# Kernel tuning notes

Hardware: AMD Instinct MI355X
Metric: run time of the kernel (lower is better)

Reference implementation:

```python
import jax, jax.numpy as jnp
import numpy as np

def mish(x):
    return x * jnp.tanh(jax.nn.softplus(x))

def setup_inputs() -> dict:
    ANT, RF, DS, G, B = 64, 8, 8, 16, 4096
    BB_DIM = 2 * RF * DS      # 128
    RF_DIM = 2 * ANT * RF     # 1024
    key = jax.random.key(0)
    ks = jax.random.split(key, 10)
    def lin(kw, kb, i, o):
        lim = 1.0 / np.sqrt(i)
        W = jax.random.uniform(kw, (o, i), jnp.float32, -lim, lim)
        b = jax.random.uniform(kb, (o,), jnp.float32, -lim, lim)
        return W, b
    W_rfbb, b_rfbb = lin(ks[0], ks[1], RF_DIM, BB_DIM)
    W_rfrf, b_rfrf = lin(ks[2], ks[3], RF_DIM, RF_DIM)
    W_bbrf, b_bbrf = lin(ks[4], ks[5], BB_DIM, RF_DIM)
    W_bbbb, b_bbbb = lin(ks[6], ks[7], BB_DIM, BB_DIM)
    BB_feature = jax.random.normal(ks[8], (B, G, BB_DIM), jnp.float32)
    RF_feature = jax.random.normal(ks[9], (B, RF_DIM), jnp.float32)
    return {
        "BB_feature": BB_feature, "RF_feature": RF_feature,
        "W_rfbb": W_rfbb, "b_rfbb": b_rfbb,
        "W_rfrf": W_rfrf, "b_rfrf": b_rfrf,
        "W_bbrf": W_bbrf, "b_bbrf": b_bbrf,
        "W_bbbb": W_bbbb, "b_bbbb": b_bbbb,
    }

def reference(BB_feature, RF_feature, W_rfbb, b_rfbb, W_rfrf, b_rfrf, W_bbrf, b_bbrf, W_bbbb, b_bbbb):
    # mean over subcarrier-group dim
    BB_mean = jnp.mean(BB_feature, axis=-2)                      # [B, BB_DIM]
    RF_to_RF = mish(RF_feature @ W_rfrf.T + b_rfrf)              # [B, RF_DIM]
    RF_to_BB = mish(RF_feature @ W_rfbb.T + b_rfbb)              # [B, BB_DIM]
    BB_to_RF = mish(BB_mean @ W_bbrf.T + b_bbrf)                 # [B, RF_DIM]
    BB_to_BB = mish(jnp.einsum('bgi,oi->bgo', BB_feature, W_bbbb) + b_bbbb)  # [B, G, BB_DIM]
    new_RF = RF_to_RF + BB_to_RF
    new_BB = BB_to_BB + RF_to_BB[:, None, :]
    return (new_BB, new_RF)
```

## Files before the change

### kernel.cpp

```cpp
#include <hip/hip_runtime.h>
#include <hip/hip_bf16.h>

typedef __attribute__((ext_vector_type(8))) short short8;
typedef __attribute__((ext_vector_type(4))) float floatx4;

#define BDIM 128
#define RDIM 1024
#define NB   4096
#define NG   16
#define LDP  40
#define WSTR 136

__device__ __forceinline__ float mishf(float x) {
    float e = __expf(x);
    float t = e * (e + 2.0f);
    float r = x * (t / (t + 2.0f));
    return x > 20.0f ? x : r;
}

__device__ __forceinline__ short8 cvt8v(float4 f0, float4 f1) {
    union { __hip_bfloat162 h; unsigned u; } c0, c1, c2, c3;
    c0.h = __float22bfloat162_rn(make_float2(f0.x, f0.y));
    c1.h = __float22bfloat162_rn(make_float2(f0.z, f0.w));
    c2.h = __float22bfloat162_rn(make_float2(f1.x, f1.y));
    c3.h = __float22bfloat162_rn(make_float2(f1.z, f1.w));
    union { short8 s; unsigned u[4]; } r;
    r.u[0] = c0.u; r.u[1] = c1.u; r.u[2] = c2.u; r.u[3] = c3.u;
    return r.s;
}

#define MFMA(a, b, c) __builtin_amdgcn_mfma_f32_16x16x32_bf16(a, b, c, 0, 0, 0)

__global__ void __launch_bounds__(256) k_mean(const float* __restrict__ bb,
                                              float* __restrict__ mean) {
    int tid = blockIdx.x * blockDim.x + threadIdx.x;
    int b = tid >> 5;
    int d = (tid & 31) * 4;
    const float4* p = (const float4*)(bb + (size_t)b * (NG * BDIM) + d);
    float4 s = {0.f, 0.f, 0.f, 0.f};
    #pragma unroll
    for (int g = 0; g < NG; ++g) {
        float4 v = p[g * (BDIM / 4)];
        s.x += v.x; s.y += v.y; s.z += v.z; s.w += v.w;
    }
    s.x *= 0.0625f; s.y *= 0.0625f; s.z *= 0.0625f; s.w *= 0.0625f;
    *(float4*)(mean + (size_t)b * BDIM + d) = s;
}

__global__ void __launch_bounds__(256) k_newrf(
    const float* __restrict__ rf,
    const float* __restrict__ meanp,
    const float* __restrict__ Wrfrf,
    const float* __restrict__ brfrf,
    const float* __restrict__ Wbbrf,
    const float* __restrict__ bbbrf,
    const float* __restrict__ Wrfbb,
    const float* __restrict__ brfbb,
    float* __restrict__ out,
    float* __restrict__ rf2bb)
{
    __shared__ short As[2][128 * LDP];
    __shared__ short Bs[2][64 * LDP];
    __shared__ short Ws2[2][16 * LDP];
    int tid = threadIdx.x;
    int wave = tid >> 6, lane = tid & 63;
    int r = lane & 15, quad = lane >> 4;
    int wm = (wave & 1) * 64, wn = (wave >> 1) * 32;
    int mt = blockIdx.x >> 4, nt = blockIdx.x & 15;
    int m0 = mt * 128, n0 = nt * 64;
    bool doP = (nt < 8);

    int arow = tid >> 1, akh = (tid & 1) * 16;
    int brow = tid >> 2, bkq = (tid & 3) * 8;
    int aidx = arow * LDP + akh;
    int bidx = brow * LDP + bkq;
    int widx = (tid >> 2) * LDP + bkq;

    const float* aG = rf    + (size_t)(m0 + arow) * RDIM + akh;
    const float* bG = Wrfrf + (size_t)(n0 + brow) * RDIM + bkq;
    const float* wG = Wrfbb + (size_t)(nt * 16 + (tid >> 2)) * RDIM + bkq;

    floatx4 acc1[4][2], acc2[4][2], acc3[4];
    #pragma unroll
    for (int mi = 0; mi < 4; ++mi) {
        acc1[mi][0] = floatx4{0.f,0.f,0.f,0.f}; acc1[mi][1] = acc1[mi][0];
        acc2[mi][0] = acc1[mi][0]; acc2[mi][1] = acc1[mi][0];
        acc3[mi] = acc1[mi][0];
    }
    float4 ra0, ra1, ra2, ra3, rb0, rb1, rw0, rw1;
    bool wload = doP && (tid < 64);

    ra0 = ((const float4*)aG)[0]; ra1 = ((const float4*)aG)[1];
    ra2 = ((const float4*)aG)[2]; ra3 = ((const float4*)aG)[3];
    rb0 = ((const float4*)bG)[0]; rb1 = ((const float4*)bG)[1];
    if (wload) { rw0 = ((const float4*)wG)[0]; rw1 = ((const float4*)wG)[1]; }
    *(short8*)&As[0][aidx]     = cvt8v(ra0, ra1);
    *(short8*)&As[0][aidx + 8] = cvt8v(ra2, ra3);
    *(short8*)&Bs[0][bidx]     = cvt8v(rb0, rb1);
    if (wload) *(short8*)&Ws2[0][widx] = cvt8v(rw0, rw1);
    ra0 = ((const float4*)(aG + 32))[0]; ra1 = ((const float4*)(aG + 32))[1];
    ra2 = ((const float4*)(aG + 32))[2]; ra3 = ((const float4*)(aG + 32))[3];
    rb0 = ((const float4*)(bG + 32))[0]; rb1 = ((const float4*)(bG + 32))[1];
    if (wload) { rw0 = ((const float4*)(wG + 32))[0]; rw1 = ((const float4*)(wG + 32))[1]; }
    __syncthreads();

    for (int it = 0; it < 32; ++it) {
        const short* Ac = As[it & 1];
        const short* Bc = Bs[it & 1];
        const short* Wc = Ws2[it & 1];
        short8 af[4];
        #pragma unroll
        for (int mi = 0; mi < 4; ++mi)
            af[mi] = *(const short8*)&Ac[(wm + mi * 16 + r) * LDP + quad * 8];
        short8 bf[2];
        bf[0] = *(const short8*)&Bc[(wn + r) * LDP + quad * 8];
        bf[1] = *(const short8*)&Bc[(wn + 16 + r) * LDP + quad * 8];
        #pragma unroll
        for (int mi = 0; mi < 4; ++mi) {
            acc1[mi][0] = MFMA(af[mi], bf[0], acc1[mi][0]);
            acc1[mi][1] = MFMA(af[mi], bf[1], acc1[mi][1]);
        }
        if (doP && (wave & 2) == 0) {
            short8 b2 = *(const short8*)&Wc[r * LDP + quad * 8];
            #pragma unroll
            for (int mi = 0; mi < 4; ++mi) acc3[mi] = MFMA(af[mi], b2, acc3[mi]);
        }
        if (it < 31) {
            int nb = (it + 1) & 1;
            *(short8*)&As[nb][aidx]     = cvt8v(ra0, ra1);
            *(short8*)&As[nb][aidx + 8] = cvt8v(ra2, ra3);
            *(short8*)&Bs[nb][bidx]     = cvt8v(rb0, rb1);
            if (wload) *(short8*)&Ws2[nb][widx] = cvt8v(rw0, rw1);
        }
        if (it < 30) {
            int k = (it + 2) * 32;
            ra0 = ((const float4*)(aG + k))[0]; ra1 = ((const float4*)(aG + k))[1];
            ra2 = ((const float4*)(aG + k))[2]; ra3 = ((const float4*)(aG + k))[3];
            rb0 = ((const float4*)(bG + k))[0]; rb1 = ((const float4*)(bG + k))[1];
            if (wload) { rw0 = ((const float4*)(wG + k))[0]; rw1 = ((const float4*)(wG + k))[1]; }
        }
        __syncthreads();
    }

    const float* a2G = meanp + (size_t)(m0 + arow) * BDIM + akh;
    const float* b2G = Wbbrf + (size_t)(n0 + brow) * BDIM + bkq;
    ra0 = ((const float4*)a2G)[0]; ra1 = ((const float4*)a2G)[1];
    ra2 = ((const float4*)a2G)[2]; ra3 = ((const float4*)a2G)[3];
    rb0 = ((const float4*)b2G)[0]; rb1 = ((const float4*)b2G)[1];
    *(short8*)&As[0][aidx]     = cvt8v(ra0, ra1);
    *(short8*)&As[0][aidx + 8] = cvt8v(ra2, ra3);
    *(short8*)&Bs[0][bidx]     = cvt8v(rb0, rb1);
    ra0 = ((const float4*)(a2G + 32))[0]; ra1 = ((const float4*)(a2G + 32))[1];
    ra2 = ((const float4*)(a2G + 32))[2]; ra3 = ((const float4*)(a2G + 32))[3];
    rb0 = ((const float4*)(b2G + 32))[0]; rb1 = ((const float4*)(b2G + 32))[1];
    __syncthreads();
    for (int it = 0; it < 4; ++it) {
        const short* Ac = As[it & 1];
        const short* Bc = Bs[it & 1];
        short8 af[4];
        #pragma unroll
        for (int mi = 0; mi < 4; ++mi)
            af[mi] = *(const short8*)&Ac[(wm + mi * 16 + r) * LDP + quad * 8];
        short8 bf[2];
        bf[0] = *(const short8*)&Bc[(wn + r) * LDP + quad * 8];
        bf[1] = *(const short8*)&Bc[(wn + 16 + r) * LDP + quad * 8];
        #pragma unroll
        for (int mi = 0; mi < 4; ++mi) {
            acc2[mi][0] = MFMA(af[mi], bf[0], acc2[mi][0]);
            acc2[mi][1] = MFMA(af[mi], bf[1], acc2[mi][1]);
        }
        if (it < 3) {
            int nb = (it + 1) & 1;
            *(short8*)&As[nb][aidx]     = cvt8v(ra0, ra1);
            *(short8*)&As[nb][aidx + 8] = cvt8v(ra2, ra3);
            *(short8*)&Bs[nb][bidx]     = cvt8v(rb0, rb1);
        }
        if (it < 2) {
            int k = (it + 2) * 32;
            ra0 = ((const float4*)(a2G + k))[0]; ra1 = ((const float4*)(a2G + k))[1];
            ra2 = ((const float4*)(a2G + k))[2]; ra3 = ((const float4*)(a2G + k))[3];
            rb0 = ((const float4*)(b2G + k))[0]; rb1 = ((const float4*)(b2G + k))[1];
        }
        __syncthreads();
    }

    #pragma unroll
    for (int nj = 0; nj < 2; ++nj) {
        int col = n0 + wn + nj * 16 + r;
        float b1 = brfrf[col];
        float b2 = bbbrf[col];
        #pragma unroll
        for (int mi = 0; mi < 4; ++mi) {
            #pragma unroll
            for (int g = 0; g < 4; ++g) {
                int row = m0 + wm + mi * 16 + quad * 4 + g;
                out[(size_t)row * RDIM + col] =
                    mishf(acc1[mi][nj][g] + b1) + mishf(acc2[mi][nj][g] + b2);
            }
        }
    }
    if (doP && (wave & 2) == 0) {
        int col = nt * 16 + r;
        float bs = brfbb[col];
        #pragma unroll
        for (int mi = 0; mi < 4; ++mi) {
            #pragma unroll
            for (int g = 0; g < 4; ++g) {
                int row = m0 + wm + mi * 16 + quad * 4 + g;
                rf2bb[(size_t)row * BDIM + col] = mishf(acc3[mi][g] + bs);
            }
        }
    }
}

__global__ void __launch_bounds__(256) k_newbb(
    const float* __restrict__ bb,
    const float* __restrict__ W,
    const float* __restrict__ bias,
    const float* __restrict__ rf2bb,
    float* __restrict__ out)
{
    __shared__ short Wt[128 * WSTR];
    __shared__ short As[2][128 * LDP];
    int tid = threadIdx.x;
    int wave = tid >> 6, lane = tid & 63;
    int r = lane & 15, quad = lane >> 4;
    size_t m0 = (size_t)blockIdx.x * 128;

    {
        int row = tid >> 1, half = (tid & 1) * 64;
        const float* wp = W + (size_t)row * BDIM + half;
        #pragma unroll
        for (int j = 0; j < 8; ++j) {
            float4 f0 = ((const float4*)(wp + j * 8))[0];
            float4 f1 = ((const float4*)(wp + j * 8))[1];
            *(short8*)&Wt[row * WSTR + half + j * 8] = cvt8v(f0, f1);
        }
    }

    int arow = tid >> 1, akh = (tid & 1) * 16;
    int aidx = arow * LDP + akh;
    const float* aG = bb + (m0 + arow) * BDIM + akh;

    floatx4 acc[2][8];
    #pragma unroll
    for (int i = 0; i < 2; ++i)
        #pragma unroll
        for (int j = 0; j < 8; ++j) acc[i][j] = floatx4{0.f,0.f,0.f,0.f};

    float4 ra0, ra1, ra2, ra3;
    ra0 = ((const float4*)aG)[0]; ra1 = ((const float4*)aG)[1];
    ra2 = ((const float4*)aG)[2]; ra3 = ((const float4*)aG)[3];
    *(short8*)&As[0][aidx]     = cvt8v(ra0, ra1);
    *(short8*)&As[0][aidx + 8] = cvt8v(ra2, ra3);
    ra0 = ((const float4*)(aG + 32))[0]; ra1 = ((const float4*)(aG + 32))[1];
    ra2 = ((const float4*)(aG + 32))[2]; ra3 = ((const float4*)(aG + 32))[3];
    __syncthreads();

    for (int kc = 0; kc < 4; ++kc) {
        const short* Ac = As[kc & 1];
        short8 a0 = *(const short8*)&Ac[(wave * 32 + r) * LDP + quad * 8];
        short8 a1 = *(const short8*)&Ac[(wave * 32 + 16 + r) * LDP + quad * 8];
        #pragma unroll
        for (int nj = 0; nj < 8; ++nj) {
            short8 b = *(const short8*)&Wt[(nj * 16 + r) * WSTR + kc * 32 + quad * 8];
            acc[0][nj] = MFMA(a0, b, acc[0][nj]);
            acc[1][nj] = MFMA(a1, b, acc[1][nj]);
        }
        if (kc < 3) {
            int nb = (kc + 1) & 1;
            *(short8*)&As[nb][aidx]     = cvt8v(ra0, ra1);
            *(short8*)&As[nb][aidx + 8] = cvt8v(ra2, ra3);
        }
        if (kc < 2) {
            int k = (kc + 2) * 32;
            ra0 = ((const float4*)(aG + k))[0]; ra1 = ((const float4*)(aG + k))[1];
            ra2 = ((const float4*)(aG + k))[2]; ra3 = ((const float4*)(aG + k))[3];
        }
        __syncthreads();
    }

    #pragma unroll
    for (int mi = 0; mi < 2; ++mi) {
        #pragma unroll
        for (int nj = 0; nj < 8; ++nj) {
            int col = nj * 16 + r;
            float bs = bias[col];
            #pragma unroll
            for (int g = 0; g < 4; ++g) {
                size_t row = m0 + wave * 32 + mi * 16 + quad * 4 + g;
                out[row * BDIM + col] = mishf(acc[mi][nj][g] + bs) + rf2bb[(row >> 4) * BDIM + col];
            }
        }
    }
}

extern "C" void kernel_launch(void* const* d_in, const int* in_sizes, int n_in,
                              void* d_out, int out_size, void* d_ws, size_t ws_size,
                              hipStream_t stream) {
    const float* BB    = (const float*)d_in[0];
    const float* RF    = (const float*)d_in[1];
    const float* Wrfbb = (const float*)d_in[2];
    const float* brfbb = (const float*)d_in[3];
    const float* Wrfrf = (const float*)d_in[4];
    const float* brfrf = (const float*)d_in[5];
    const float* Wbbrf = (const float*)d_in[6];
    const float* bbbrf = (const float*)d_in[7];
    const float* Wbbbb = (const float*)d_in[8];
    const float* bbbbb = (const float*)d_in[9];

    float* outBB = (float*)d_out;
    float* outRF = outBB + (size_t)NB * NG * BDIM;

    float* mean  = (float*)d_ws;
    float* rf2bb = (float*)((char*)d_ws + (size_t)NB * BDIM * 4);

    k_mean <<<512, 256, 0, stream>>>(BB, mean);
    k_newrf<<<512, 256, 0, stream>>>(RF, mean, Wrfrf, brfrf, Wbbrf, bbbrf,
                                     Wrfbb, brfbb, outRF, rf2bb);
    k_newbb<<<512, 256, 0, stream>>>(BB, Wbbbb, bbbbb, rf2bb, outBB);
}
```

Baseline: 164.6 us.

## Pre-convert inputs to bf16 and stage GEMM tiles with direct global-to-LDS loads

```diff
diff --git a/kernel.cpp b/kernel.cpp
--- a/kernel.cpp
+++ b/kernel.cpp
@@ -2,14 +2,13 @@
 #include <hip/hip_bf16.h>
 
 typedef __attribute__((ext_vector_type(8))) short short8;
+typedef __attribute__((ext_vector_type(4))) short short4v;
 typedef __attribute__((ext_vector_type(4))) float floatx4;
 
 #define BDIM 128
 #define RDIM 1024
 #define NB   4096
 #define NG   16
-#define LDP  40
-#define WSTR 136
 
 __device__ __forceinline__ float mishf(float x) {
     float e = __expf(x);
@@ -29,39 +28,85 @@
     return r.s;
 }
 
+__device__ __forceinline__ short4v cvt4v(float4 f) {
+    union { __hip_bfloat162 h; unsigned u; } c0, c1;
+    c0.h = __float22bfloat162_rn(make_float2(f.x, f.y));
+    c1.h = __float22bfloat162_rn(make_float2(f.z, f.w));
+    union { short4v s; unsigned u[2]; } r;
+    r.u[0] = c0.u; r.u[1] = c1.u;
+    return r.s;
+}
+
+__device__ __forceinline__ void gld16(const void* g, void* l) {
+    __builtin_amdgcn_global_load_lds(
+        (const __attribute__((address_space(1))) unsigned int*)g,
+        (__attribute__((address_space(3))) unsigned int*)l, 16, 0, 0);
+}
+
 #define MFMA(a, b, c) __builtin_amdgcn_mfma_f32_16x16x32_bf16(a, b, c, 0, 0, 0)
 
-__global__ void __launch_bounds__(256) k_mean(const float* __restrict__ bb,
-                                              float* __restrict__ mean) {
-    int tid = blockIdx.x * blockDim.x + threadIdx.x;
-    int b = tid >> 5;
-    int d = (tid & 31) * 4;
-    const float4* p = (const float4*)(bb + (size_t)b * (NG * BDIM) + d);
-    float4 s = {0.f, 0.f, 0.f, 0.f};
-    #pragma unroll
-    for (int g = 0; g < NG; ++g) {
-        float4 v = p[g * (BDIM / 4)];
-        s.x += v.x; s.y += v.y; s.z += v.z; s.w += v.w;
-    }
-    s.x *= 0.0625f; s.y *= 0.0625f; s.z *= 0.0625f; s.w *= 0.0625f;
-    *(float4*)(mean + (size_t)b * BDIM + d) = s;
+#define RF_N     4194304u
+#define C1       4194304u
+#define C2       5242880u
+#define C3       5373952u
+#define C4       5505024u
+#define CT       5521408u
+
+__global__ void __launch_bounds__(256) k_prep(
+    const float* __restrict__ bb, const float* __restrict__ rf,
+    const float* __restrict__ Wrfrf, const float* __restrict__ Wrfbb,
+    const float* __restrict__ Wbbrf, const float* __restrict__ Wbbbb,
+    short* __restrict__ bb_b, short* __restrict__ mean_b, short* __restrict__ rf_b,
+    short* __restrict__ wrfrf_b, short* __restrict__ wrfbb_b,
+    short* __restrict__ wbbrf_b, short* __restrict__ wbbbb_b)
+{
+    int bid = blockIdx.x;
+    int tid = threadIdx.x;
+    if (bid < 512) {
+        int b = bid * 8 + (tid >> 5);
+        int d = (tid & 31) * 4;
+        const float4* p = (const float4*)(bb + (size_t)b * (NG * BDIM) + d);
+        short* ob = bb_b + (size_t)b * (NG * BDIM) + d;
+        float4 s = {0.f, 0.f, 0.f, 0.f};
+        #pragma unroll
+        for (int g = 0; g < NG; ++g) {
+            float4 v = p[g * (BDIM / 4)];
+            s.x += v.x; s.y += v.y; s.z += v.z; s.w += v.w;
+            *(short4v*)(ob + g * BDIM) = cvt4v(v);
+        }
+        s.x *= 0.0625f; s.y *= 0.0625f; s.z *= 0.0625f; s.w *= 0.0625f;
+        *(short4v*)(mean_b + (size_t)b * BDIM + d) = cvt4v(s);
+    } else {
+        size_t t = (size_t)(bid - 512) * 256 + tid;
+        for (size_t base = t * 8; base < CT; base += (size_t)512 * 256 * 8) {
+            const float* s; short* dst; size_t off;
+            if (base < C1)      { s = rf;    dst = rf_b;    off = base; }
+            else if (base < C2) { s = Wrfrf; dst = wrfrf_b; off = base - C1; }
+            else if (base < C3) { s = Wrfbb; dst = wrfbb_b; off = base - C2; }
+            else if (base < C4) { s = Wbbrf; dst = wbbrf_b; off = base - C3; }
+            else                { s = Wbbbb; dst = wbbbb_b; off = base - C4; }
+            float4 f0 = ((const float4*)(s + off))[0];
+            float4 f1 = ((const float4*)(s + off))[1];
+            *(short8*)(dst + off) = cvt8v(f0, f1);
+        }
+    }
 }
 
 __global__ void __launch_bounds__(256) k_newrf(
-    const float* __restrict__ rf,
-    const float* __restrict__ meanp,
-    const float* __restrict__ Wrfrf,
+    const short* __restrict__ rfb,
+    const short* __restrict__ meanb,
+    const short* __restrict__ wrfrfb,
     const float* __restrict__ brfrf,
-    const float* __restrict__ Wbbrf,
+    const short* __restrict__ wbbrfb,
     const float* __restrict__ bbbrf,
-    const float* __restrict__ Wrfbb,
+    const short* __restrict__ wrfbbb,
     const float* __restrict__ brfbb,
     float* __restrict__ out,
     float* __restrict__ rf2bb)
 {
-    __shared__ short As[2][128 * LDP];
-    __shared__ short Bs[2][64 * LDP];
-    __shared__ short Ws2[2][16 * LDP];
+    __shared__ alignas(16) short As[2][128 * 64];
+    __shared__ alignas(16) short Bs[2][64 * 64];
+    __shared__ alignas(16) short Ws2[2][16 * 64];
     int tid = threadIdx.x;
     int wave = tid >> 6, lane = tid & 63;
     int r = lane & 15, quad = lane >> 4;
@@ -70,15 +115,12 @@
     int m0 = mt * 128, n0 = nt * 64;
     bool doP = (nt < 8);
 
-    int arow = tid >> 1, akh = (tid & 1) * 16;
-    int brow = tid >> 2, bkq = (tid & 3) * 8;
-    int aidx = arow * LDP + akh;
-    int bidx = brow * LDP + bkq;
-    int widx = (tid >> 2) * LDP + bkq;
-
-    const float* aG = rf    + (size_t)(m0 + arow) * RDIM + akh;
-    const float* bG = Wrfrf + (size_t)(n0 + brow) * RDIM + bkq;
-    const float* wG = Wrfbb + (size_t)(nt * 16 + (tid >> 2)) * RDIM + bkq;
+    int srow = lane >> 3;
+    int scol = ((lane & 7) ^ srow) * 8;
+
+    const short* aB = rfb    + (size_t)(m0 + wave * 32 + srow) * RDIM + scol;
+    const short* bB = wrfrfb + (size_t)(n0 + wave * 16 + srow) * RDIM + scol;
+    const short* wB = wrfbbb + (size_t)(nt * 16 + srow) * RDIM + scol;
 
     floatx4 acc1[4][2], acc2[4][2], acc3[4];
     #pragma unroll
@@ -87,99 +129,84 @@
         acc2[mi][0] = acc1[mi][0]; acc2[mi][1] = acc1[mi][0];
         acc3[mi] = acc1[mi][0];
     }
-    float4 ra0, ra1, ra2, ra3, rb0, rb1, rw0, rw1;
-    bool wload = doP && (tid < 64);
-
-    ra0 = ((const float4*)aG)[0]; ra1 = ((const float4*)aG)[1];
-    ra2 = ((const float4*)aG)[2]; ra3 = ((const float4*)aG)[3];
-    rb0 = ((const float4*)bG)[0]; rb1 = ((const float4*)bG)[1];
-    if (wload) { rw0 = ((const float4*)wG)[0]; rw1 = ((const float4*)wG)[1]; }
-    *(short8*)&As[0][aidx]     = cvt8v(ra0, ra1);
-    *(short8*)&As[0][aidx + 8] = cvt8v(ra2, ra3);
-    *(short8*)&Bs[0][bidx]     = cvt8v(rb0, rb1);
-    if (wload) *(short8*)&Ws2[0][widx] = cvt8v(rw0, rw1);
-    ra0 = ((const float4*)(aG + 32))[0]; ra1 = ((const float4*)(aG + 32))[1];
-    ra2 = ((const float4*)(aG + 32))[2]; ra3 = ((const float4*)(aG + 32))[3];
-    rb0 = ((const float4*)(bG + 32))[0]; rb1 = ((const float4*)(bG + 32))[1];
-    if (wload) { rw0 = ((const float4*)(wG + 32))[0]; rw1 = ((const float4*)(wG + 32))[1]; }
+
+    auto stage1 = [&](int buf, int k) {
+        #pragma unroll
+        for (int j = 0; j < 4; ++j)
+            gld16(aB + (size_t)j * 8 * RDIM + k, &As[buf][(wave * 32 + j * 8) * 64]);
+        #pragma unroll
+        for (int j = 0; j < 2; ++j)
+            gld16(bB + (size_t)j * 8 * RDIM + k, &Bs[buf][(wave * 16 + j * 8) * 64]);
+        if (doP && wave == 0) {
+            #pragma unroll
+            for (int j = 0; j < 2; ++j)
+                gld16(wB + (size_t)j * 8 * RDIM + k, &Ws2[buf][j * 8 * 64]);
+        }
+    };
+
+    stage1(0, 0);
     __syncthreads();
 
-    for (int it = 0; it < 32; ++it) {
-        const short* Ac = As[it & 1];
-        const short* Bc = Bs[it & 1];
-        const short* Wc = Ws2[it & 1];
-        short8 af[4];
-        #pragma unroll
-        for (int mi = 0; mi < 4; ++mi)
-            af[mi] = *(const short8*)&Ac[(wm + mi * 16 + r) * LDP + quad * 8];
-        short8 bf[2];
-        bf[0] = *(const short8*)&Bc[(wn + r) * LDP + quad * 8];
-        bf[1] = *(const short8*)&Bc[(wn + 16 + r) * LDP + quad * 8];
-        #pragma unroll
-        for (int mi = 0; mi < 4; ++mi) {
-            acc1[mi][0] = MFMA(af[mi], bf[0], acc1[mi][0]);
-            acc1[mi][1] = MFMA(af[mi], bf[1], acc1[mi][1]);
-        }
-        if (doP && (wave & 2) == 0) {
-            short8 b2 = *(const short8*)&Wc[r * LDP + quad * 8];
-            #pragma unroll
-            for (int mi = 0; mi < 4; ++mi) acc3[mi] = MFMA(af[mi], b2, acc3[mi]);
-        }
-        if (it < 31) {
-            int nb = (it + 1) & 1;
-            *(short8*)&As[nb][aidx]     = cvt8v(ra0, ra1);
-            *(short8*)&As[nb][aidx + 8] = cvt8v(ra2, ra3);
-            *(short8*)&Bs[nb][bidx]     = cvt8v(rb0, rb1);
-            if (wload) *(short8*)&Ws2[nb][widx] = cvt8v(rw0, rw1);
-        }
-        if (it < 30) {
-            int k = (it + 2) * 32;
-            ra0 = ((const float4*)(aG + k))[0]; ra1 = ((const float4*)(aG + k))[1];
-            ra2 = ((const float4*)(aG + k))[2]; ra3 = ((const float4*)(aG + k))[3];
-            rb0 = ((const float4*)(bG + k))[0]; rb1 = ((const float4*)(bG + k))[1];
-            if (wload) { rw0 = ((const float4*)(wG + k))[0]; rw1 = ((const float4*)(wG + k))[1]; }
+    for (int it = 0; it < 16; ++it) {
+        int buf = it & 1;
+        if (it < 15) stage1(buf ^ 1, (it + 1) * 64);
+        const short* Ac = As[buf];
+        const short* Bc = Bs[buf];
+        const short* Wc = Ws2[buf];
+        #pragma unroll
+        for (int kk = 0; kk < 2; ++kk) {
+            int sw = (((kk << 2) + quad) ^ (r & 7)) << 3;
+            short8 af[4];
+            #pragma unroll
+            for (int mi = 0; mi < 4; ++mi)
+                af[mi] = *(const short8*)&Ac[(wm + mi * 16 + r) * 64 + sw];
+            short8 bf0 = *(const short8*)&Bc[(wn + r) * 64 + sw];
+            short8 bf1 = *(const short8*)&Bc[(wn + 16 + r) * 64 + sw];
+            #pragma unroll
+            for (int mi = 0; mi < 4; ++mi) {
+                acc1[mi][0] = MFMA(af[mi], bf0, acc1[mi][0]);
+                acc1[mi][1] = MFMA(af[mi], bf1, acc1[mi][1]);
+            }
+            if (doP && (wave & 2) == 0) {
+                short8 b2 = *(const short8*)&Wc[r * 64 + sw];
+                #pragma unroll
+                for (int mi = 0; mi < 4; ++mi) acc3[mi] = MFMA(af[mi], b2, acc3[mi]);
+            }
         }
         __syncthreads();
     }
 
-    const float* a2G = meanp + (size_t)(m0 + arow) * BDIM + akh;
-    const float* b2G = Wbbrf + (size_t)(n0 + brow) * BDIM + bkq;
-    ra0 = ((const float4*)a2G)[0]; ra1 = ((const float4*)a2G)[1];
-    ra2 = ((const float4*)a2G)[2]; ra3 = ((const float4*)a2G)[3];
-    rb0 = ((const float4*)b2G)[0]; rb1 = ((const float4*)b2G)[1];
-    *(short8*)&As[0][aidx]     = cvt8v(ra0, ra1);
-    *(short8*)&As[0][aidx + 8] = cvt8v(ra2, ra3);
-    *(short8*)&Bs[0][bidx]     = cvt8v(rb0, rb1);
-    ra0 = ((const float4*)(a2G + 32))[0]; ra1 = ((const float4*)(a2G + 32))[1];
-    ra2 = ((const float4*)(a2G + 32))[2]; ra3 = ((const float4*)(a2G + 32))[3];
-    rb0 = ((const float4*)(b2G + 32))[0]; rb1 = ((const float4*)(b2G + 32))[1];
+    const short* a2B = meanb  + (size_t)(m0 + wave * 32 + srow) * BDIM + scol;
+    const short* b2B = wbbrfb + (size_t)(n0 + wave * 16 + srow) * BDIM + scol;
+    auto stage2 = [&](int buf, int k) {
+        #pragma unroll
+        for (int j = 0; j < 4; ++j)
+            gld16(a2B + (size_t)j * 8 * BDIM + k, &As[buf][(wave * 32 + j * 8) * 64]);
+        #pragma unroll
+        for (int j = 0; j < 2; ++j)
+            gld16(b2B + (size_t)j * 8 * BDIM + k, &Bs[buf][(wave * 16 + j * 8) * 64]);
+    };
+    stage2(0, 0);
     __syncthreads();
-    for (int it = 0; it < 4; ++it) {
-        const short* Ac = As[it & 1];
-        const short* Bc = Bs[it & 1];
-        short8 af[4];
-        #pragma unroll
-        for (int mi = 0; mi < 4; ++mi)
-            af[mi] = *(const short8*)&Ac[(wm + mi * 16 + r) * LDP + quad * 8];
-        short8 bf[2];
-        bf[0] = *(const short8*)&Bc[(wn + r) * LDP + quad * 8];
-        bf[1] = *(const short8*)&Bc[(wn + 16 + r) * LDP + quad * 8];
-        #pragma unroll
-        for (int mi = 0; mi < 4; ++mi) {
-            acc2[mi][0] = MFMA(af[mi], bf[0], acc2[mi][0]);
-            acc2[mi][1] = MFMA(af[mi], bf[1], acc2[mi][1]);
-        }
-        if (it < 3) {
-            int nb = (it + 1) & 1;
-            *(short8*)&As[nb][aidx]     = cvt8v(ra0, ra1);
-            *(short8*)&As[nb][aidx + 8] = cvt8v(ra2, ra3);
-            *(short8*)&Bs[nb][bidx]     = cvt8v(rb0, rb1);
-        }
-        if (it < 2) {
-            int k = (it + 2) * 32;
-            ra0 = ((const float4*)(a2G + k))[0]; ra1 = ((const float4*)(a2G + k))[1];
-            ra2 = ((const float4*)(a2G + k))[2]; ra3 = ((const float4*)(a2G + k))[3];
-            rb0 = ((const float4*)(b2G + k))[0]; rb1 = ((const float4*)(b2G + k))[1];
+    for (int it = 0; it < 2; ++it) {
+        int buf = it & 1;
+        if (it < 1) stage2(1, 64);
+        const short* Ac = As[buf];
+        const short* Bc = Bs[buf];
+        #pragma unroll
+        for (int kk = 0; kk < 2; ++kk) {
+            int sw = (((kk << 2) + quad) ^ (r & 7)) << 3;
+            short8 af[4];
+            #pragma unroll
+            for (int mi = 0; mi < 4; ++mi)
+                af[mi] = *(const short8*)&Ac[(wm + mi * 16 + r) * 64 + sw];
+            short8 bf0 = *(const short8*)&Bc[(wn + r) * 64 + sw];
+            short8 bf1 = *(const short8*)&Bc[(wn + 16 + r) * 64 + sw];
+            #pragma unroll
+            for (int mi = 0; mi < 4; ++mi) {
+                acc2[mi][0] = MFMA(af[mi], bf0, acc2[mi][0]);
+                acc2[mi][1] = MFMA(af[mi], bf1, acc2[mi][1]);
+            }
         }
         __syncthreads();
     }
@@ -214,33 +241,28 @@
 }
 
 __global__ void __launch_bounds__(256) k_newbb(
-    const float* __restrict__ bb,
-    const float* __restrict__ W,
+    const short* __restrict__ bbb,
+    const short* __restrict__ wb,
     const float* __restrict__ bias,
     const float* __restrict__ rf2bb,
     float* __restrict__ out)
 {
-    __shared__ short Wt[128 * WSTR];
-    __shared__ short As[2][128 * LDP];
+    __shared__ alignas(16) short At[128 * 128];
+    __shared__ alignas(16) short Wt[128 * 128];
     int tid = threadIdx.x;
     int wave = tid >> 6, lane = tid & 63;
     int r = lane & 15, quad = lane >> 4;
     size_t m0 = (size_t)blockIdx.x * 128;
 
-    {
-        int row = tid >> 1, half = (tid & 1) * 64;
-        const float* wp = W + (size_t)row * BDIM + half;
-        #pragma unroll
-        for (int j = 0; j < 8; ++j) {
-            float4 f0 = ((const float4*)(wp + j * 8))[0];
-            float4 f1 = ((const float4*)(wp + j * 8))[1];
-            *(short8*)&Wt[row * WSTR + half + j * 8] = cvt8v(f0, f1);
-        }
-    }
-
-    int arow = tid >> 1, akh = (tid & 1) * 16;
-    int aidx = arow * LDP + akh;
-    const float* aG = bb + (m0 + arow) * BDIM + akh;
+    int lrow = lane >> 4;
+    int lslot = lane & 15;
+    #pragma unroll
+    for (int j = 0; j < 8; ++j) {
+        int row = wave * 32 + j * 4 + lrow;
+        int col = ((lslot ^ (row & 7)) << 3);
+        gld16(bbb + (m0 + row) * BDIM + col, &At[(wave * 32 + j * 4) * 128]);
+        gld16(wb + (size_t)row * BDIM + col,  &Wt[(wave * 32 + j * 4) * 128]);
+    }
 
     floatx4 acc[2][8];
     #pragma unroll
@@ -248,36 +270,19 @@
         #pragma unroll
         for (int j = 0; j < 8; ++j) acc[i][j] = floatx4{0.f,0.f,0.f,0.f};
 
-    float4 ra0, ra1, ra2, ra3;
-    ra0 = ((const float4*)aG)[0]; ra1 = ((const float4*)aG)[1];
-    ra2 = ((const float4*)aG)[2]; ra3 = ((const float4*)aG)[3];
-    *(short8*)&As[0][aidx]     = cvt8v(ra0, ra1);
-    *(short8*)&As[0][aidx + 8] = cvt8v(ra2, ra3);
-    ra0 = ((const float4*)(aG + 32))[0]; ra1 = ((const float4*)(aG + 32))[1];
-    ra2 = ((const float4*)(aG + 32))[2]; ra3 = ((const float4*)(aG + 32))[3];
     __syncthreads();
 
+    #pragma unroll
     for (int kc = 0; kc < 4; ++kc) {
-        const short* Ac = As[kc & 1];
-        short8 a0 = *(const short8*)&Ac[(wave * 32 + r) * LDP + quad * 8];
-        short8 a1 = *(const short8*)&Ac[(wave * 32 + 16 + r) * LDP + quad * 8];
+        int sw = (((kc << 2) + quad) ^ (r & 7)) << 3;
+        short8 a0 = *(const short8*)&At[(wave * 32 + r) * 128 + sw];
+        short8 a1 = *(const short8*)&At[(wave * 32 + 16 + r) * 128 + sw];
         #pragma unroll
         for (int nj = 0; nj < 8; ++nj) {
-            short8 b = *(const short8*)&Wt[(nj * 16 + r) * WSTR + kc * 32 + quad * 8];
+            short8 b = *(const short8*)&Wt[(nj * 16 + r) * 128 + sw];
             acc[0][nj] = MFMA(a0, b, acc[0][nj]);
             acc[1][nj] = MFMA(a1, b, acc[1][nj]);
         }
-        if (kc < 3) {
-            int nb = (kc + 1) & 1;
-            *(short8*)&As[nb][aidx]     = cvt8v(ra0, ra1);
-            *(short8*)&As[nb][aidx + 8] = cvt8v(ra2, ra3);
-        }
-        if (kc < 2) {
-            int k = (kc + 2) * 32;
-            ra0 = ((const float4*)(aG + k))[0]; ra1 = ((const float4*)(aG + k))[1];
-            ra2 = ((const float4*)(aG + k))[2]; ra3 = ((const float4*)(aG + k))[3];
-        }
-        __syncthreads();
     }
 
     #pragma unroll
@@ -312,11 +317,20 @@
     float* outBB = (float*)d_out;
     float* outRF = outBB + (size_t)NB * NG * BDIM;
 
-    float* mean  = (float*)d_ws;
-    float* rf2bb = (float*)((char*)d_ws + (size_t)NB * BDIM * 4);
-
-    k_mean <<<512, 256, 0, stream>>>(BB, mean);
-    k_newrf<<<512, 256, 0, stream>>>(RF, mean, Wrfrf, brfrf, Wbbrf, bbbrf,
-                                     Wrfbb, brfbb, outRF, rf2bb);
-    k_newbb<<<512, 256, 0, stream>>>(BB, Wbbbb, bbbbb, rf2bb, outBB);
-}
+    char* w = (char*)d_ws;
+    short* mean_b  = (short*)(w);
+    short* rf_b    = (short*)(w + 1048576);
+    short* wrfrf_b = (short*)(w + 9437184);
+    short* wrfbb_b = (short*)(w + 11534336);
+    short* wbbrf_b = (short*)(w + 11796480);
+    short* wbbbb_b = (short*)(w + 12058624);
+    short* bb_b    = (short*)(w + 12091392);
+    float* rf2bb   = (float*)(w + 28868608);
+
+    k_prep <<<1024, 256, 0, stream>>>(BB, RF, Wrfrf, Wrfbb, Wbbrf, Wbbbb,
+                                      bb_b, mean_b, rf_b, wrfrf_b, wrfbb_b,
+                                      wbbrf_b, wbbbb_b);
+    k_newrf<<<512, 256, 0, stream>>>(rf_b, mean_b, wrfrf_b, brfrf, wbbrf_b, bbbrf,
+                                     wrfbb_b, brfbb, outRF, rf2bb);
+    k_newbb<<<512, 256, 0, stream>>>(bb_b, wbbbb_b, bbbbb, rf2bb, outBB);
+}
```

New measurement: 153.0 us. 1.08x faster.
